# Kernel tuning notes

Measured on AMD Instinct MI355X. Metric: run time of the kernel, lower is better.

## Reference

```python
import jax, jax.numpy as jnp
import numpy as np

HEAD_NUM = 16
HEAD_DIM = 128
INPUT_DIM = 1024
OUTPUT_DIM = 1024


def setup_inputs() -> dict:
    key = jax.random.key(0)
    k1, k2, k3 = jax.random.split(key, 3)
    x = jax.random.normal(k1, (64, 512, INPUT_DIM), dtype=jnp.float32)
    # Linear weights stored as (in, out); torch Linear computes x @ W.T, so this
    # is equivalent with W = torch_weight.T. Scaled like default init.
    W_pre = jax.random.normal(k2, (INPUT_DIM, 3 * HEAD_NUM * HEAD_DIM), dtype=jnp.float32) * (1.0 / np.sqrt(INPUT_DIM))
    b_pre = jnp.zeros((3 * HEAD_NUM * HEAD_DIM,), dtype=jnp.float32)
    W_proj = jax.random.normal(k3, (HEAD_DIM, OUTPUT_DIM), dtype=jnp.float32) * (1.0 / np.sqrt(HEAD_DIM))
    b_proj = jnp.zeros((OUTPUT_DIM,), dtype=jnp.float32)
    return {"x": x, "W_pre": W_pre, "b_pre": b_pre, "W_proj": W_proj, "b_proj": b_proj}


def reference(x, W_pre, b_pre, W_proj, b_proj):
    old_shape = x.shape[:-1]
    B = int(np.prod(old_shape))
    xf = x.reshape(B, INPUT_DIM)
    qkv = xf @ W_pre + b_pre                      # [B, 3*H*D]
    q, k, v = jnp.split(qkv, 3, axis=1)
    q = q.reshape(B, HEAD_NUM, HEAD_DIM)
    k = k.reshape(B, HEAD_NUM, HEAD_DIM)
    v = v.reshape(B, HEAD_NUM, HEAD_DIM)
    # attention across heads (head_num acts as the sequence axis)
    score = jnp.einsum('bhd,bgd->bhg', q, k) / np.sqrt(HEAD_DIM)  # [B, H, H]
    score = jax.nn.softmax(score, axis=2)
    att = jnp.einsum('bhg,bgd->bhd', score, v)    # [B, H, D]
    proj = jnp.einsum('bhd,do->bho', att, W_proj) + b_proj        # [B, H, O]
    out = proj.sum(axis=1)                        # [B, O]
    return out.reshape(*old_shape, OUTPUT_DIM)
```

## Files before the change

kernel.cpp:

```cpp
#include <hip/hip_runtime.h>

#define H        16
#define HD       128
#define IN_DIM   1024
#define QKV_DIM  6144
#define OUT_DIM  1024
#define B_TOTAL  32768
#define CHUNK    8192
#define NCHUNK   4

typedef unsigned short u16;
typedef __attribute__((ext_vector_type(8))) __bf16 bf16x8;
typedef __attribute__((ext_vector_type(4))) float  f32x4;

__device__ __forceinline__ u16 f2bf(float f) {
  unsigned u = __float_as_uint(f);
  u += 0x7fff + ((u >> 16) & 1);
  return (u16)(u >> 16);
}
__device__ __forceinline__ float bf2f(u16 s) {
  return __uint_as_float(((unsigned)s) << 16);
}

#define GLDS16(gp, lp) __builtin_amdgcn_global_load_lds( \
    (__attribute__((address_space(1))) void*)(gp), \
    (__attribute__((address_space(3))) void*)(lp), 16, 0, 0)

__global__ void cvt_x(const float* __restrict__ src, u16* __restrict__ dst, int n8) {
  int stride = gridDim.x * blockDim.x;
  for (int i = blockIdx.x * blockDim.x + threadIdx.x; i < n8; i += stride) {
    const float4* s = (const float4*)(src + (size_t)i * 8);
    float4 f0 = s[0], f1 = s[1];
    ushort4 o0, o1;
    o0.x = f2bf(f0.x); o0.y = f2bf(f0.y); o0.z = f2bf(f0.z); o0.w = f2bf(f0.w);
    o1.x = f2bf(f1.x); o1.y = f2bf(f1.y); o1.z = f2bf(f1.z); o1.w = f2bf(f1.w);
    *(ushort4*)(dst + (size_t)i * 8)     = o0;
    *(ushort4*)(dst + (size_t)i * 8 + 4) = o1;
  }
}

__global__ void transpose_cvt(const float* __restrict__ src, u16* __restrict__ dst,
                              int R, int C) {
  __shared__ float tile[32][33];
  int tx = threadIdx.x & 31, ty = threadIdx.x >> 5;
  int c0 = blockIdx.x * 32, r0 = blockIdx.y * 32;
  #pragma unroll
  for (int i = 0; i < 32; i += 8)
    tile[ty + i][tx] = src[(size_t)(r0 + ty + i) * C + c0 + tx];
  __syncthreads();
  #pragma unroll
  for (int i = 0; i < 32; i += 8)
    dst[(size_t)(c0 + ty + i) * R + r0 + tx] = f2bf(tile[tx][ty + i]);
}

__global__ void gemm1(const u16* __restrict__ A, const u16* __restrict__ BT,
                      const float* __restrict__ bias, u16* __restrict__ Cq) {
  __shared__ u16 As[128 * 32];
  __shared__ u16 Bs[128 * 32];
  int tid = threadIdx.x;
  int lane = tid & 63, wave = tid >> 6;
  int wm = wave >> 1, wn = wave & 1;
  int m0 = blockIdx.y * 128, n0 = blockIdx.x * 128;

  f32x4 zero = {0.f, 0.f, 0.f, 0.f};
  f32x4 acc[4][4];
  #pragma unroll
  for (int m = 0; m < 4; ++m)
    #pragma unroll
    for (int n = 0; n < 4; ++n) acc[m][n] = zero;

  for (int k0 = 0; k0 < IN_DIM; k0 += 32) {
    #pragma unroll
    for (int i = 0; i < 2; ++i) {
      int idx = i * 256 + tid;
      int row = idx >> 2, kc = (idx & 3) * 8;
      GLDS16(A  + (size_t)(m0 + row) * IN_DIM + k0 + kc, As + (size_t)(i * 256 + wave * 64) * 8);
      GLDS16(BT + (size_t)(n0 + row) * IN_DIM + k0 + kc, Bs + (size_t)(i * 256 + wave * 64) * 8);
    }
    __syncthreads();
    bf16x8 af[4], bv[4];
    #pragma unroll
    for (int m = 0; m < 4; ++m)
      af[m] = *(const bf16x8*)&As[(wm * 64 + m * 16 + (lane & 15)) * 32 + (lane >> 4) * 8];
    #pragma unroll
    for (int n = 0; n < 4; ++n)
      bv[n] = *(const bf16x8*)&Bs[(wn * 64 + n * 16 + (lane & 15)) * 32 + (lane >> 4) * 8];
    #pragma unroll
    for (int m = 0; m < 4; ++m)
      #pragma unroll
      for (int n = 0; n < 4; ++n)
        acc[m][n] = __builtin_amdgcn_mfma_f32_16x16x32_bf16(af[m], bv[n], acc[m][n], 0, 0, 0);
    __syncthreads();
  }

  int rbase = m0 + wm * 64 + (lane >> 4) * 4;
  int cbase = n0 + wn * 64 + (lane & 15);
  #pragma unroll
  for (int m = 0; m < 4; ++m)
    #pragma unroll
    for (int n = 0; n < 4; ++n) {
      int ccol = cbase + n * 16;
      float bb = bias[ccol];
      #pragma unroll
      for (int j = 0; j < 4; ++j) {
        int rr = rbase + m * 16 + j;
        Cq[(size_t)rr * QKV_DIM + ccol] = f2bf(acc[m][n][j] + bb);
      }
    }
}

__global__ void attn(const u16* __restrict__ qkv, u16* __restrict__ attsum) {
  int wave = threadIdx.x >> 6, lane = threadIdx.x & 63;
  int b = blockIdx.x * 4 + wave;
  const u16* q = qkv + (size_t)b * QKV_DIM;
  const u16* k = q + H * HD;
  const u16* v = q + 2 * H * HD;

  int hr = lane & 15, kc = (lane >> 4) * 8;
  f32x4 sc = {0.f, 0.f, 0.f, 0.f};
  #pragma unroll
  for (int s = 0; s < 4; ++s) {
    bf16x8 aq = *(const bf16x8*)&q[hr * HD + s * 32 + kc];
    bf16x8 ak = *(const bf16x8*)&k[hr * HD + s * 32 + kc];
    sc = __builtin_amdgcn_mfma_f32_16x16x32_bf16(aq, ak, sc, 0, 0, 0);
  }
  const float scale = 0.08838834764831845f;
  float w = 0.f;
  #pragma unroll
  for (int j = 0; j < 4; ++j) {
    float xv = sc[j] * scale;
    float mx = xv;
    #pragma unroll
    for (int d = 1; d < 16; d <<= 1) mx = fmaxf(mx, __shfl_xor(mx, d));
    float e = __expf(xv - mx);
    float s = e;
    #pragma unroll
    for (int d = 1; d < 16; d <<= 1) s += __shfl_xor(s, d);
    w += e / s;
  }
  w += __shfl_xor(w, 16);
  w += __shfl_xor(w, 32);

  float a0 = 0.f, a1 = 0.f;
  #pragma unroll
  for (int g = 0; g < 16; ++g) {
    float wg = __shfl(w, g);
    a0 += wg * bf2f(v[g * HD + lane]);
    a1 += wg * bf2f(v[g * HD + 64 + lane]);
  }
  attsum[(size_t)b * HD + lane]      = f2bf(a0);
  attsum[(size_t)b * HD + 64 + lane] = f2bf(a1);
}

__global__ void gemm2(const u16* __restrict__ A, const u16* __restrict__ BT,
                      const float* __restrict__ bias, float* __restrict__ out) {
  __shared__ u16 As[128 * 128];
  __shared__ u16 Bs[128 * 128];
  int tid = threadIdx.x, lane = tid & 63, wave = tid >> 6;
  int wm = wave >> 1, wn = wave & 1;
  int m0 = blockIdx.y * 128, n0 = blockIdx.x * 128;

  #pragma unroll
  for (int i = 0; i < 8; ++i) {
    int idx = i * 256 + tid;
    int row = idx >> 4, kc = (idx & 15) * 8;
    GLDS16(A  + (size_t)(m0 + row) * HD + kc, As + (size_t)(i * 256 + wave * 64) * 8);
    GLDS16(BT + (size_t)(n0 + row) * HD + kc, Bs + (size_t)(i * 256 + wave * 64) * 8);
  }
  __syncthreads();

  f32x4 zero = {0.f, 0.f, 0.f, 0.f};
  f32x4 acc[4][4];
  #pragma unroll
  for (int m = 0; m < 4; ++m)
    #pragma unroll
    for (int n = 0; n < 4; ++n) acc[m][n] = zero;

  #pragma unroll
  for (int s = 0; s < 4; ++s) {
    bf16x8 af[4], bv[4];
    #pragma unroll
    for (int m = 0; m < 4; ++m)
      af[m] = *(const bf16x8*)&As[(wm * 64 + m * 16 + (lane & 15)) * HD + s * 32 + (lane >> 4) * 8];
    #pragma unroll
    for (int n = 0; n < 4; ++n)
      bv[n] = *(const bf16x8*)&Bs[(wn * 64 + n * 16 + (lane & 15)) * HD + s * 32 + (lane >> 4) * 8];
    #pragma unroll
    for (int m = 0; m < 4; ++m)
      #pragma unroll
      for (int n = 0; n < 4; ++n)
        acc[m][n] = __builtin_amdgcn_mfma_f32_16x16x32_bf16(af[m], bv[n], acc[m][n], 0, 0, 0);
  }

  int rbase = m0 + wm * 64 + (lane >> 4) * 4;
  int cbase = n0 + wn * 64 + (lane & 15);
  #pragma unroll
  for (int m = 0; m < 4; ++m)
    #pragma unroll
    for (int n = 0; n < 4; ++n) {
      int ccol = cbase + n * 16;
      float bb = 16.f * bias[ccol];
      #pragma unroll
      for (int j = 0; j < 4; ++j) {
        int rr = rbase + m * 16 + j;
        out[(size_t)rr * OUT_DIM + ccol] = acc[m][n][j] + bb;
      }
    }
}

extern "C" void kernel_launch(void* const* d_in, const int* in_sizes, int n_in,
                              void* d_out, int out_size, void* d_ws, size_t ws_size,
                              hipStream_t stream) {
  const float* x      = (const float*)d_in[0];
  const float* W_pre  = (const float*)d_in[1];
  const float* b_pre  = (const float*)d_in[2];
  const float* W_proj = (const float*)d_in[3];
  const float* b_proj = (const float*)d_in[4];
  float* out = (float*)d_out;

  u16* wpreT  = (u16*)d_ws;
  u16* wprojT = wpreT  + (size_t)QKV_DIM * IN_DIM;
  u16* xb     = wprojT + (size_t)OUT_DIM * HD;
  u16* qkvb   = xb     + (size_t)CHUNK * IN_DIM;
  u16* attb   = qkvb   + (size_t)CHUNK * QKV_DIM;

  transpose_cvt<<<dim3(QKV_DIM / 32, IN_DIM / 32), 256, 0, stream>>>(W_pre, wpreT, IN_DIM, QKV_DIM);
  transpose_cvt<<<dim3(OUT_DIM / 32, HD / 32), 256, 0, stream>>>(W_proj, wprojT, HD, OUT_DIM);

  for (int c = 0; c < NCHUNK; ++c) {
    const float* xc = x + (size_t)c * CHUNK * IN_DIM;
    cvt_x<<<1024, 256, 0, stream>>>(xc, xb, CHUNK * IN_DIM / 8);
    gemm1<<<dim3(QKV_DIM / 128, CHUNK / 128), 256, 0, stream>>>(xb, wpreT, b_pre, qkvb);
    attn<<<CHUNK / 4, 256, 0, stream>>>(qkvb, attb);
    gemm2<<<dim3(OUT_DIM / 128, CHUNK / 128), 256, 0, stream>>>(attb, wprojT, b_proj,
                                                                out + (size_t)c * CHUNK * OUT_DIM);
  }
}
```

Before: 815.2 us.

## Rewrite QKV GEMM with 256x256 tiles, double-buffered swizzled LDS and phased scheduling

Replaces the simple 128x128 single-buffer QKV GEMM with a 256x256 tile, 512-thread kernel. It double-buffers LDS with a BK of 64 and XOR-swizzles LDS rows to avoid bank conflicts. Each iteration is split into phases that interleave async global->LDS loads, LDS->register loads and MFMA work, using explicit barriers, waitcnts and setprio. The goal is to hide memory latency and raise MFMA utilisation in the dominant GEMM, at the cost of high register and LDS pressure (128 KB LDS per block) and fragile hand scheduling.

```diff
diff --git a/kernel.cpp b/kernel.cpp
--- a/kernel.cpp
+++ b/kernel.cpp
@@ -53,60 +53,120 @@
     dst[(size_t)(c0 + ty + i) * R + r0 + tx] = f2bf(tile[tx][ty + i]);
 }
 
-__global__ void gemm1(const u16* __restrict__ A, const u16* __restrict__ BT,
-                      const float* __restrict__ bias, u16* __restrict__ Cq) {
-  __shared__ u16 As[128 * 32];
-  __shared__ u16 Bs[128 * 32];
-  int tid = threadIdx.x;
-  int lane = tid & 63, wave = tid >> 6;
-  int wm = wave >> 1, wn = wave & 1;
-  int m0 = blockIdx.y * 128, n0 = blockIdx.x * 128;
-
-  f32x4 zero = {0.f, 0.f, 0.f, 0.f};
-  f32x4 acc[4][4];
-  #pragma unroll
-  for (int m = 0; m < 4; ++m)
-    #pragma unroll
-    for (int n = 0; n < 4; ++n) acc[m][n] = zero;
-
-  for (int k0 = 0; k0 < IN_DIM; k0 += 32) {
-    #pragma unroll
-    for (int i = 0; i < 2; ++i) {
-      int idx = i * 256 + tid;
-      int row = idx >> 2, kc = (idx & 3) * 8;
-      GLDS16(A  + (size_t)(m0 + row) * IN_DIM + k0 + kc, As + (size_t)(i * 256 + wave * 64) * 8);
-      GLDS16(BT + (size_t)(n0 + row) * IN_DIM + k0 + kc, Bs + (size_t)(i * 256 + wave * 64) * 8);
-    }
-    __syncthreads();
-    bf16x8 af[4], bv[4];
-    #pragma unroll
-    for (int m = 0; m < 4; ++m)
-      af[m] = *(const bf16x8*)&As[(wm * 64 + m * 16 + (lane & 15)) * 32 + (lane >> 4) * 8];
-    #pragma unroll
-    for (int n = 0; n < 4; ++n)
-      bv[n] = *(const bf16x8*)&Bs[(wn * 64 + n * 16 + (lane & 15)) * 32 + (lane >> 4) * 8];
-    #pragma unroll
-    for (int m = 0; m < 4; ++m)
+
+#define PH(ds, stg, wait, mm) do { ds; stg; \
+    __builtin_amdgcn_sched_barrier(0); \
+    __builtin_amdgcn_s_barrier(); \
+    asm volatile("s_waitcnt lgkmcnt(0)" ::: "memory"); \
+    __builtin_amdgcn_sched_barrier(0); \
+    __builtin_amdgcn_s_setprio(1); mm; __builtin_amdgcn_s_setprio(0); \
+    wait; \
+    __builtin_amdgcn_sched_barrier(0); \
+    __builtin_amdgcn_s_barrier(); } while (0)
+
+#define VM(n) asm volatile("s_waitcnt vmcnt(" #n ")" ::: "memory")
+#define NOP ((void)0)
+
+#define LDA(buf, mhalf) do { \
+    _Pragma("unroll") for (int mf_ = 0; mf_ < 4; ++mf_) { \
+      int row_ = wm * 128 + (mhalf) * 64 + mf_ * 16 + l15; \
+      int sw_ = (row_ & 7) << 3; \
+      _Pragma("unroll") for (int kk_ = 0; kk_ < 2; ++kk_) \
+        areg[mf_][kk_] = *(const bf16x8*)&As[buf][row_ * 64 + ((kk_ * 32 + l4x8) ^ sw_)]; \
+    } } while (0)
+
+#define LDB(buf, nhalf) do { \
+    _Pragma("unroll") for (int nf_ = 0; nf_ < 2; ++nf_) { \
+      int row_ = wn * 64 + (nhalf) * 32 + nf_ * 16 + l15; \
+      int sw_ = (row_ & 7) << 3; \
+      _Pragma("unroll") for (int kk_ = 0; kk_ < 2; ++kk_) \
+        breg[nhalf][nf_][kk_] = *(const bf16x8*)&Bs[buf][row_ * 64 + ((kk_ * 32 + l4x8) ^ sw_)]; \
+    } } while (0)
+
+#define MM(mhalf, nhalf) do { \
+    _Pragma("unroll") for (int kk_ = 0; kk_ < 2; ++kk_) \
+    _Pragma("unroll") for (int mf_ = 0; mf_ < 4; ++mf_) \
+    _Pragma("unroll") for (int nf_ = 0; nf_ < 2; ++nf_) \
+      acc[(mhalf) * 4 + mf_][(nhalf) * 2 + nf_] = __builtin_amdgcn_mfma_f32_16x16x32_bf16( \
+          areg[mf_][kk_], breg[nhalf][nf_][kk_], acc[(mhalf) * 4 + mf_][(nhalf) * 2 + nf_], 0, 0, 0); \
+    } while (0)
+
+#define STA(buf, half, kt) do { \
+    const u16* g_ = A + (size_t)(m0 + (half) * 128) * IN_DIM + (kt) * 64; \
+    _Pragma("unroll") for (int ld_ = 0; ld_ < 2; ++ld_) { \
+      int idx_ = ld_ * 512 + tid; int row_ = idx_ >> 3, g8_ = idx_ & 7; \
+      int scol_ = (g8_ ^ (row_ & 7)) * 8; \
+      GLDS16(g_ + (size_t)row_ * IN_DIM + scol_, \
+             &As[buf][(half) * 8192 + (ld_ * 512 + wave * 64) * 8]); \
+    } } while (0)
+
+#define STB(buf, half, kt) do { \
+    const u16* g_ = BT + (size_t)(n0 + (half) * 128) * IN_DIM + (kt) * 64; \
+    _Pragma("unroll") for (int ld_ = 0; ld_ < 2; ++ld_) { \
+      int idx_ = ld_ * 512 + tid; int row_ = idx_ >> 3, g8_ = idx_ & 7; \
+      int scol_ = (g8_ ^ (row_ & 7)) * 8; \
+      GLDS16(g_ + (size_t)row_ * IN_DIM + scol_, \
+             &Bs[buf][(half) * 8192 + (ld_ * 512 + wave * 64) * 8]); \
+    } } while (0)
+
+__global__ __launch_bounds__(512, 2)
+void gemm1(const u16* __restrict__ A, const u16* __restrict__ BT,
+           const float* __restrict__ bias, u16* __restrict__ Cq) {
+  __shared__ u16 As[2][256 * 64];
+  __shared__ u16 Bs[2][256 * 64];
+  int tid = threadIdx.x, lane = tid & 63, wave = tid >> 6;
+  int wm = wave >> 2, wn = wave & 3;
+  int l15 = lane & 15, l4x8 = (lane >> 4) * 8;
+  int m0 = blockIdx.y * 256, n0 = blockIdx.x * 256;
+
+  f32x4 acc[8][4];
+  #pragma unroll
+  for (int m = 0; m < 8; ++m)
+    #pragma unroll
+    for (int n = 0; n < 4; ++n) acc[m][n] = (f32x4){0.f, 0.f, 0.f, 0.f};
+
+  bf16x8 areg[4][2];
+  bf16x8 breg[2][2][2];
+
+  STB(0, 0, 0); STB(0, 1, 0);
+  STA(0, 0, 0); STA(0, 1, 0);
+  STB(1, 0, 1); STB(1, 1, 1);
+  VM(4);
+  __builtin_amdgcn_sched_barrier(0);
+  __builtin_amdgcn_s_barrier();
+
+  for (int it = 0; it < 7; ++it) {
+    int t = 2 * it;
+    PH( { LDA(0, 0); LDB(0, 0); }, STA(1, 0, t + 1), NOP,   MM(0, 0) );
+    PH( { LDB(0, 1); },            STA(1, 1, t + 1), NOP,   MM(0, 1) );
+    PH( { LDA(0, 1); },            STB(0, 0, t + 2), NOP,   MM(1, 0) );
+    PH( NOP,                       STB(0, 1, t + 2), VM(4), MM(1, 1) );
+    PH( { LDA(1, 0); LDB(1, 0); }, STA(0, 0, t + 2), NOP,   MM(0, 0) );
+    PH( { LDB(1, 1); },            STA(0, 1, t + 2), NOP,   MM(0, 1) );
+    PH( { LDA(1, 1); },            STB(1, 0, t + 3), NOP,   MM(1, 0) );
+    PH( NOP,                       STB(1, 1, t + 3), VM(4), MM(1, 1) );
+  }
+  PH( { LDA(0, 0); LDB(0, 0); }, STA(1, 0, 15), NOP,   MM(0, 0) );
+  PH( { LDB(0, 1); },            STA(1, 1, 15), NOP,   MM(0, 1) );
+  PH( { LDA(0, 1); },            NOP,           NOP,   MM(1, 0) );
+  PH( NOP,                       NOP,           VM(0), MM(1, 1) );
+  PH( { LDA(1, 0); LDB(1, 0); }, NOP,           NOP,   MM(0, 0) );
+  PH( { LDB(1, 1); },            NOP,           NOP,   MM(0, 1) );
+  PH( { LDA(1, 1); },            NOP,           NOP,   MM(1, 0) );
+  MM(1, 1);
+
+  int rb = m0 + wm * 128 + (lane >> 4) * 4;
+  int cb = n0 + wn * 64 + l15;
+  #pragma unroll
+  for (int nf = 0; nf < 4; ++nf) {
+    int col = cb + nf * 16;
+    float bb = bias[col];
+    #pragma unroll
+    for (int mf = 0; mf < 8; ++mf)
       #pragma unroll
-      for (int n = 0; n < 4; ++n)
-        acc[m][n] = __builtin_amdgcn_mfma_f32_16x16x32_bf16(af[m], bv[n], acc[m][n], 0, 0, 0);
-    __syncthreads();
-  }
-
-  int rbase = m0 + wm * 64 + (lane >> 4) * 4;
-  int cbase = n0 + wn * 64 + (lane & 15);
-  #pragma unroll
-  for (int m = 0; m < 4; ++m)
-    #pragma unroll
-    for (int n = 0; n < 4; ++n) {
-      int ccol = cbase + n * 16;
-      float bb = bias[ccol];
-      #pragma unroll
-      for (int j = 0; j < 4; ++j) {
-        int rr = rbase + m * 16 + j;
-        Cq[(size_t)rr * QKV_DIM + ccol] = f2bf(acc[m][n][j] + bb);
-      }
-    }
+      for (int j = 0; j < 4; ++j)
+        Cq[(size_t)(rb + mf * 16 + j) * QKV_DIM + col] = f2bf(acc[mf][nf][j] + bb);
+  }
 }
 
 __global__ void attn(const u16* __restrict__ qkv, u16* __restrict__ attsum) {
@@ -154,8 +214,8 @@
 
 __global__ void gemm2(const u16* __restrict__ A, const u16* __restrict__ BT,
                       const float* __restrict__ bias, float* __restrict__ out) {
-  __shared__ u16 As[128 * 128];
-  __shared__ u16 Bs[128 * 128];
+  __shared__ u16 As2[128 * 128];
+  __shared__ u16 Bs2[128 * 128];
   int tid = threadIdx.x, lane = tid & 63, wave = tid >> 6;
   int wm = wave >> 1, wn = wave & 1;
   int m0 = blockIdx.y * 128, n0 = blockIdx.x * 128;
@@ -164,8 +224,8 @@
   for (int i = 0; i < 8; ++i) {
     int idx = i * 256 + tid;
     int row = idx >> 4, kc = (idx & 15) * 8;
-    GLDS16(A  + (size_t)(m0 + row) * HD + kc, As + (size_t)(i * 256 + wave * 64) * 8);
-    GLDS16(BT + (size_t)(n0 + row) * HD + kc, Bs + (size_t)(i * 256 + wave * 64) * 8);
+    GLDS16(A  + (size_t)(m0 + row) * HD + kc, As2 + (size_t)(i * 256 + wave * 64) * 8);
+    GLDS16(BT + (size_t)(n0 + row) * HD + kc, Bs2 + (size_t)(i * 256 + wave * 64) * 8);
   }
   __syncthreads();
 
@@ -181,10 +241,10 @@
     bf16x8 af[4], bv[4];
     #pragma unroll
     for (int m = 0; m < 4; ++m)
-      af[m] = *(const bf16x8*)&As[(wm * 64 + m * 16 + (lane & 15)) * HD + s * 32 + (lane >> 4) * 8];
+      af[m] = *(const bf16x8*)&As2[(wm * 64 + m * 16 + (lane & 15)) * HD + s * 32 + (lane >> 4) * 8];
     #pragma unroll
     for (int n = 0; n < 4; ++n)
-      bv[n] = *(const bf16x8*)&Bs[(wn * 64 + n * 16 + (lane & 15)) * HD + s * 32 + (lane >> 4) * 8];
+      bv[n] = *(const bf16x8*)&Bs2[(wn * 64 + n * 16 + (lane & 15)) * HD + s * 32 + (lane >> 4) * 8];
     #pragma unroll
     for (int m = 0; m < 4; ++m)
       #pragma unroll
@@ -230,7 +290,7 @@
   for (int c = 0; c < NCHUNK; ++c) {
     const float* xc = x + (size_t)c * CHUNK * IN_DIM;
     cvt_x<<<1024, 256, 0, stream>>>(xc, xb, CHUNK * IN_DIM / 8);
-    gemm1<<<dim3(QKV_DIM / 128, CHUNK / 128), 256, 0, stream>>>(xb, wpreT, b_pre, qkvb);
+    gemm1<<<dim3(QKV_DIM / 256, CHUNK / 256), 512, 0, stream>>>(xb, wpreT, b_pre, qkvb);
     attn<<<CHUNK / 4, 256, 0, stream>>>(qkvb, attb);
     gemm2<<<dim3(OUT_DIM / 128, CHUNK / 128), 256, 0, stream>>>(attb, wprojT, b_proj,
                                                                 out + (size_t)c * CHUNK * OUT_DIM);
```

Result: no change. 831.4 us (+2.0%).
